# Optimization experiments

Measured on AMD Instinct MI355X. Metric: run time of the kernel, lower is better.

Reference implementation:

```python
import jax, jax.numpy as jnp
import numpy as np
from jax.ops import segment_sum, segment_max

N, E, G = 50000, 500000, 64
H1, C = 4, 64  # gat1 heads, per-head dim; gat2 has 1 head
NEG_SLOPE = 0.2


def setup_inputs() -> dict:
    key = jax.random.key(0)
    ks = jax.random.split(key, 30)
    rn = lambda k, sh, s=0.1: (jax.random.normal(k, sh, dtype=jnp.float32) * s)
    inp = {
        'x': rn(ks[0], (N, 5), 1.0),
        'edge_attr': rn(ks[1], (E, 2), 1.0),
        'edge_index': jax.random.randint(ks[2], (2, E), 0, N),
        'batch': jnp.sort(jax.random.randint(ks[3], (N,), 0, G)),
        # gat1: lin_l/lin_r (5->256), lin_edge (2->256, no bias), att [4,64], out bias [256]
        'Wl1': rn(ks[4], (5, H1 * C)), 'bl1': rn(ks[5], (H1 * C,)),
        'Wr1': rn(ks[6], (5, H1 * C)), 'br1': rn(ks[7], (H1 * C,)),
        'We1': rn(ks[8], (2, H1 * C)), 'att1': rn(ks[9], (H1, C)), 'bias1': rn(ks[10], (H1 * C,)),
        # gat2: 256->64, 1 head
        'Wl2': rn(ks[11], (H1 * C, C)), 'bl2': rn(ks[12], (C,)),
        'Wr2': rn(ks[13], (H1 * C, C)), 'br2': rn(ks[14], (C,)),
        'We2': rn(ks[15], (2, C)), 'att2': rn(ks[16], (1, C)), 'bias2': rn(ks[17], (C,)),
        # GRU (input 64, hidden 64), torch gate order r,z,n; stored as [in,3H]/[H,3H]
        'Wi': rn(ks[18], (C, 3 * C)), 'Wh': rn(ks[19], (C, 3 * C)),
        'bi': rn(ks[20], (3 * C,)), 'bh': rn(ks[21], (3 * C,)),
        # classifier 64->32->1
        'Wc1': rn(ks[22], (C, 32)), 'bc1': rn(ks[23], (32,)),
        'Wc2': rn(ks[24], (32, 1)), 'bc2': rn(ks[25], (1,)),
    }
    return inp


def _add_self_loops(edge_index, edge_attr):
    # PyG default: add_self_loops=True, fill_value='mean' -> self-loop edge_attr is
    # the mean of incoming edge attrs at each destination node (0 if none).
    src, dst = edge_index[0], edge_index[1]
    deg = segment_sum(jnp.ones((E,), jnp.float32), dst, num_segments=N)
    mean_attr = segment_sum(edge_attr, dst, num_segments=N) / jnp.maximum(deg, 1.0)[:, None]
    loop = jnp.arange(N)
    return (jnp.concatenate([src, loop]), jnp.concatenate([dst, loop]),
            jnp.concatenate([edge_attr, mean_attr], axis=0))


def _segment_softmax(logits, dst):
    # logits: [E', H]; softmax over edges sharing the same destination
    m = segment_max(logits, dst, num_segments=N)
    ex = jnp.exp(logits - m[dst])
    s = segment_sum(ex, dst, num_segments=N)
    return ex / s[dst]


def _gatv2(x, src, dst, eattr, Wl, bl, Wr, br, We, att, bias, H):
    n = x.shape[0]
    xl = (x @ Wl + bl).reshape(n, H, C)  # messages from source
    xr = (x @ Wr + br).reshape(n, H, C)  # destination term
    e = (eattr @ We).reshape(-1, H, C)
    msg = xl[src] + xr[dst] + e  # [E',H,C]
    logits = jnp.einsum('ehc,hc->eh', jax.nn.leaky_relu(msg, NEG_SLOPE), att)
    alpha = _segment_softmax(logits, dst)  # [E',H]
    out = segment_sum(xl[src] * alpha[:, :, None], dst, num_segments=N)  # [N,H,C]
    return out.reshape(n, H * C) + bias


def _gru_last(seq, Wi, Wh, bi, bh):
    # seq: [T, C] (torch GRU with batch=1); returns last hidden state [C]
    def step(h, xt):
        gi = xt @ Wi + bi
        gh = h @ Wh + bh
        ir, iz, inn = jnp.split(gi, 3)
        hr, hz, hn = jnp.split(gh, 3)
        r = jax.nn.sigmoid(ir + hr)
        z = jax.nn.sigmoid(iz + hz)
        nn_ = jnp.tanh(inn + r * hn)
        h_new = (1.0 - z) * nn_ + z * h
        return h_new, None
    h0 = jnp.zeros((C,), seq.dtype)
    hT, _ = jax.lax.scan(step, h0, seq)
    return hT


def reference(x, edge_attr, Wl1, bl1, Wr1, br1, We1, att1, bias1,
              Wl2, bl2, Wr2, br2, We2, att2, bias2,
              Wi, Wh, bi, bh, Wc1, bc1, Wc2, bc2, edge_index, batch):
    src, dst, ea = _add_self_loops(edge_index, edge_attr)
    h = jax.nn.elu(_gatv2(x, src, dst, ea, Wl1, bl1, Wr1, br1, We1, att1, bias1, H1))
    h = jax.nn.elu(_gatv2(h, src, dst, ea, Wl2, bl2, Wr2, br2, We2, att2, bias2, 1))
    # global mean pool over graphs
    cnt = segment_sum(jnp.ones((N,), h.dtype), batch, num_segments=G)
    pooled = segment_sum(h, batch, num_segments=G) / jnp.maximum(cnt, 1.0)[:, None]  # [G,C]
    hT = _gru_last(pooled, Wi, Wh, bi, bh)  # [C]
    z = jax.nn.relu(hT[None, :] @ Wc1 + bc1)
    return jax.nn.sigmoid(z @ Wc2 + bc2)  # [1,1]
```

## Files before the change

kernel.cpp:

```cpp
#include <hip/hip_runtime.h>
#include <hip/hip_bf16.h>

#define NN 50000
#define EE 500000
#define EP 550000
#define GG 64

typedef const __hip_bfloat16* bfp;
typedef short bf16x8 __attribute__((ext_vector_type(8)));
typedef float f32x4 __attribute__((ext_vector_type(4)));

__device__ __forceinline__ int clampN(int v) { return (int)(((unsigned)v) % (unsigned)NN); }

__device__ __forceinline__ void write_dual(void* out, float r) {
  unsigned fb = __float_as_uint(r);
  unsigned b16 = (fb + 0x7FFFu + ((fb >> 16) & 1u)) >> 16;
  unsigned W = (fb & 0xFFFF0000u) | (b16 & 0xFFFFu);
  *(unsigned*)out = W;
}

__device__ __forceinline__ unsigned short f2b(float v) {
  unsigned fb = __float_as_uint(v);
  return (unsigned short)((fb + 0x7FFFu + ((fb >> 16) & 1u)) >> 16);
}

__device__ __forceinline__ float b2f(unsigned short u) {
  return __uint_as_float(((unsigned)u) << 16);
}

#define DPP_ADD(x, ctrl) \
  ((x) + __int_as_float(__builtin_amdgcn_update_dpp(0, __float_as_int(x), ctrl, 0xF, 0xF, true)))

__device__ __forceinline__ float row_red16(float v) {
  v = DPP_ADD(v, 0xB1);
  v = DPP_ADD(v, 0x4E);
  v = DPP_ADD(v, 0x141);
  v = DPP_ADD(v, 0x140);
  return v;
}

__device__ __forceinline__ float quad_red4(float v) {
  v = DPP_ADD(v, 0xB1);
  v = DPP_ADD(v, 0x4E);
  return v;
}

__device__ __forceinline__ float cross_row(float v) {
  v += __int_as_float(__builtin_amdgcn_ds_swizzle(__float_as_int(v), 0x401F));
  v += __shfl_xor(v, 32, 64);
  return v;
}

__device__ __forceinline__ float rlane(float v, int l) {
  return __int_as_float(__builtin_amdgcn_readlane(__float_as_int(v), l));
}

__global__ void k_probe_v7(const unsigned short* xraw, int* flag) {
  if (threadIdx.x != 0 || blockIdx.x != 0) return;
  int cnt = 0;
  for (int i = 0; i < 64; i++) {
    unsigned u = ((unsigned)xraw[i]) << 16;
    float v = __uint_as_float(u);
    float a = fabsf(v);
    if (a >= 1e-5f && a <= 100.f) cnt++;
  }
  flag[0] = (cnt >= 56) ? 1 : 0;
}

struct Cvt24 {
  const void* src[24];
  float* dst[24];
  int start[25];
};

__global__ void k_cvtall_v8(Cvt24 d, const int* flag, int total) {
  int idx = blockIdx.x * 256 + threadIdx.x;
  if (idx >= total) return;
  int lo = 0, hi = 24;
  while (hi - lo > 1) {
    int mid = (lo + hi) >> 1;
    if (idx >= d.start[mid]) lo = mid; else hi = mid;
  }
  int i = idx - d.start[lo];
  if (flag[0]) d.dst[lo][i] = __bfloat162float(((bfp)d.src[lo])[i]);
  else         d.dst[lo][i] = ((const float*)d.src[lo])[i];
}

__global__ void k_zero_v7(int* p, int n) {
  int i = blockIdx.x * 256 + threadIdx.x;
  if (i < n) p[i] = 0;
}

__global__ void k_count_v7(const int* ei, const float* ea, int* deg, float* asum) {
  int e = blockIdx.x * 256 + threadIdx.x;
  if (e >= EE) return;
  int dst = clampN(ei[EE + e]);
  atomicAdd(&deg[dst], 1);
  atomicAdd(&asum[2 * dst],     ea[2 * e]);
  atomicAdd(&asum[2 * dst + 1], ea[2 * e + 1]);
}

__global__ void k_scan_v7(const int* deg, int* offs) {
  __shared__ int part[256];
  int t = threadIdx.x;
  int npt = (NN + 255) / 256;
  int lo = t * npt;
  int hi = lo + npt;
  if (hi > NN) hi = NN;
  int sum = 0;
  for (int i = lo; i < hi; i++) sum += deg[i] + 1;
  part[t] = sum;
  __syncthreads();
  for (int o = 1; o < 256; o <<= 1) {
    int add = (t >= o) ? part[t - o] : 0;
    __syncthreads();
    part[t] += add;
    __syncthreads();
  }
  int base = part[t] - sum;
  for (int i = lo; i < hi; i++) {
    offs[i] = base;
    base += deg[i] + 1;
  }
  if (t == 255) offs[NN] = part[255];
}

__global__ void k_scatter_v10(const int* ei, const float* ea,
                              const int* deg, const float* asum,
                              const int* offs, int* cursor, float4* recs) {
  int e = blockIdx.x * 256 + threadIdx.x;
  if (e >= EP) return;
  int dst, src;
  float a0, a1;
  if (e < EE) {
    dst = clampN(ei[EE + e]);
    src = clampN(ei[e]);
    a0 = ea[2 * e];
    a1 = ea[2 * e + 1];
  } else {
    dst = e - EE;
    src = dst;
    float d = (float)deg[dst];
    if (d < 1.0f) d = 1.0f;
    a0 = asum[2 * dst] / d;
    a1 = asum[2 * dst + 1] / d;
  }
  int pos = offs[dst] + atomicAdd(&cursor[dst], 1);
  if (pos >= 0 && pos < EP)
    recs[pos] = make_float4(__int_as_float(src), a0, a1, 0.f);
}

__global__ void k_packw2(const float* Wl2, const float* Wr2, unsigned short* Wp) {
  int idx = blockIdx.x * 256 + threadIdx.x;
  if (idx >= 32768) return;
  int j    = idx & 7;
  int lane = (idx >> 3) & 63;
  int nt   = (idx >> 9) & 3;
  int kt   = (idx >> 11) & 7;
  int mat  = idx >> 14;
  int k = kt * 32 + (lane >> 4) * 8 + j;
  int c = nt * 16 + (lane & 15);
  const float* W = mat ? Wr2 : Wl2;
  Wp[idx] = f2b(W[k * 64 + c]);
}

__global__ void k_gat1_v14(const float* x,
                           const float* Wl, const float* bl,
                           const float* Wr, const float* br,
                           const float* We, const float* att, const float* bias,
                           const bf16x8* Wp, const float* bl2, const float* br2,
                           const int* offs, const float4* recs,
                           unsigned short* xl2, unsigned short* xr2) {
  __shared__ __align__(16) unsigned short hS[16 * 256];
  int t = threadIdx.x;
  int w = t >> 6;
  int l = t & 63;
  int g = l >> 4;
  int m = l & 15;
  int ibase = blockIdx.x * 16;
  float wl[4][5], wr[4][5], we0v[4], we1v[4], attv[4], blv[4], brv[4], biasv[4];
#pragma unroll
  for (int q = 0; q < 4; q++) {
    int j = g * 64 + m + 16 * q;
#pragma unroll
    for (int k = 0; k < 5; k++) {
      wl[q][k] = Wl[k * 256 + j];
      wr[q][k] = Wr[k * 256 + j];
    }
    we0v[q] = We[j];
    we1v[q] = We[256 + j];
    attv[q] = att[j];
    blv[q] = bl[j];
    brv[q] = br[j];
    biasv[q] = bias[j];
  }
  for (int nn = 0; nn < 4; nn++) {
    int i = ibase + w * 4 + nn;
    if (i >= NN) break;
    float xi[5];
#pragma unroll
    for (int k = 0; k < 5; k++) xi[k] = x[i * 5 + k];
    float xrv[4];
#pragma unroll
    for (int q = 0; q < 4; q++) {
      float a = brv[q];
#pragma unroll
      for (int k = 0; k < 5; k++) a += xi[k] * wr[q][k];
      xrv[q] = a;
    }
    int p0 = offs[i], p1 = offs[i + 1];
    float s = 0.f;
    float acc[4] = {0.f, 0.f, 0.f, 0.f};
    for (int base = p0; base < p1; base += 8) {
      int rem = p1 - base;
      int idx = base + (l & 7);
      if (idx >= p1) idx = p1 - 1;
      float4 rec = recs[idx];
      float xa0 = 0.f, xa1 = 0.f, xa2 = 0.f, xa3 = 0.f, xa4 = 0.f;
      if (l < 8) {
        const float* xp = x + (size_t)__float_as_int(rec.x) * 5;
        xa0 = xp[0]; xa1 = xp[1]; xa2 = xp[2]; xa3 = xp[3]; xa4 = xp[4];
      }
#pragma unroll
      for (int j = 0; j < 8; j++) {
        if (j >= rem) break;
        float xs0 = rlane(xa0, j), xs1 = rlane(xa1, j), xs2 = rlane(xa2, j),
              xs3 = rlane(xa3, j), xs4 = rlane(xa4, j);
        float ea0 = rlane(rec.y, j), ea1 = rlane(rec.z, j);
        float xlv[4];
        float v = 0.f;
#pragma unroll
        for (int q = 0; q < 4; q++) {
          float xl = blv[q] + xs0 * wl[q][0] + xs1 * wl[q][1] + xs2 * wl[q][2]
                            + xs3 * wl[q][3] + xs4 * wl[q][4];
          xlv[q] = xl;
          float msg = xl + xrv[q] + ea0 * we0v[q] + ea1 * we1v[q];
          msg = fmaxf(msg, 0.2f * msg);
          v += msg * attv[q];
        }
        v = row_red16(v);
        float wgt = __expf(v);
        s += wgt;
#pragma unroll
        for (int q = 0; q < 4; q++) acc[q] += wgt * xlv[q];
      }
    }
    {
      int row = w * 4 + nn;
#pragma unroll
      for (int q = 0; q < 4; q++) {
        float o = acc[q] / s + biasv[q];
        o = (o > 0.f) ? o : (__expf(o) - 1.0f);
        int ch = g * 64 + m + 16 * q;
        int byte = (row * 512 + ch * 2) ^ ((row & 7) << 4);
        *(unsigned short*)((char*)hS + byte) = f2b(o);
      }
    }
  }
  __syncthreads();
  {
    int lo16 = l & 15, hi4 = l >> 4;
    f32x4 accL = {0.f, 0.f, 0.f, 0.f};
    f32x4 accR = {0.f, 0.f, 0.f, 0.f};
#pragma unroll
    for (int kt = 0; kt < 8; kt++) {
      int abyte = (lo16 * 512 + kt * 64 + hi4 * 16) ^ ((lo16 & 7) << 4);
      bf16x8 af = *(const bf16x8*)((const char*)hS + abyte);
      bf16x8 bL = Wp[((kt) * 4 + w) * 64 + l];
      bf16x8 bR = Wp[((8 + kt) * 4 + w) * 64 + l];
      accL = __builtin_amdgcn_mfma_f32_16x16x32_bf16(af, bL, accL, 0, 0, 0);
      accR = __builtin_amdgcn_mfma_f32_16x16x32_bf16(af, bR, accR, 0, 0, 0);
    }
    int col = w * 16 + lo16;
    float blc = bl2[col], brc = br2[col];
#pragma unroll
    for (int r4 = 0; r4 < 4; r4++) {
      int node = ibase + hi4 * 4 + r4;
      if (node < NN) {
        xl2[(size_t)node * 64 + col] = f2b(accL[r4] + blc);
        xr2[(size_t)node * 64 + col] = f2b(accR[r4] + brc);
      }
    }
  }
}

__global__ void k_gat2_v11(const float* We, const float* att, const float* bias,
                           const int* offs, const float4* recs,
                           const unsigned short* xl2, const unsigned short* xr2,
                           const int* batch, float* pooled_r, int* gcnt_r) {
  int i = blockIdx.x * 4 + (threadIdx.x >> 6);
  if (i >= NN) return;
  int t = threadIdx.x & 63;
  int r = t >> 4;
  int m = t & 15;
  float we0v[4], we1v[4], attv[4], xrcv[4], biasv[4];
#pragma unroll
  for (int q = 0; q < 4; q++) {
    int ch = m + 16 * q;
    we0v[q] = We[ch];
    we1v[q] = We[64 + ch];
    attv[q] = att[ch];
    biasv[q] = bias[ch];
    xrcv[q] = b2f(xr2[(size_t)i * 64 + ch]);
  }
  int p0 = offs[i], p1 = offs[i + 1];
  float s = 0.f;
  float acc[4] = {0.f, 0.f, 0.f, 0.f};
  for (int base = p0; base < p1; base += 4) {
    int eidx = base + r;
    bool valid = eidx < p1;
    float4 rec = recs[valid ? eidx : (p1 - 1)];
    const unsigned short* xlp = xl2 + (size_t)__float_as_int(rec.x) * 64;
    float xlv[4];
    float v = 0.f;
#pragma unroll
    for (int q = 0; q < 4; q++) {
      float xl = b2f(xlp[m + 16 * q]);
      xlv[q] = xl;
      float msg = xl + xrcv[q] + rec.y * we0v[q] + rec.z * we1v[q];
      msg = fmaxf(msg, 0.2f * msg);
      v += msg * attv[q];
    }
    v = row_red16(v);
    float w = valid ? __expf(v) : 0.f;
    s += w;
#pragma unroll
    for (int q = 0; q < 4; q++) acc[q] += w * xlv[q];
  }
  s = cross_row(s);
#pragma unroll
  for (int q = 0; q < 4; q++) acc[q] = cross_row(acc[q]);
  if (r == 0) {
    int gsl = (int)(((unsigned)batch[i]) % (unsigned)GG);
    int rep = i & 15;
#pragma unroll
    for (int q = 0; q < 4; q++) {
      float o = acc[q] / s + biasv[q];
      o = (o > 0.f) ? o : (__expf(o) - 1.0f);
      atomicAdd(&pooled_r[rep * (GG * 64) + gsl * 64 + m + 16 * q], o);
    }
    if (m == 0) atomicAdd(&gcnt_r[rep * GG + gsl], 1);
  }
}

__global__ void k_poolsum_v9(const float* pooled_r, const int* gcnt_r,
                             float* pooled, int* gcnt) {
  int i = blockIdx.x * 256 + threadIdx.x;
  if (i < GG * 64) {
    float a = 0.f;
    for (int r = 0; r < 16; r++) a += pooled_r[r * (GG * 64) + i];
    pooled[i] = a;
  }
  if (i < GG) {
    int a = 0;
    for (int r = 0; r < 16; r++) a += gcnt_r[r * GG + i];
    gcnt[i] = a;
  }
}

__global__ void k_gin_v7(const float* pooled, const int* gcnt,
                         const float* Wi, const float* bi, float* GI) {
  int idx = blockIdx.x * 256 + threadIdx.x;
  if (idx >= GG * 192) return;
  int ts = idx / 192;
  int j = idx % 192;
  float a = 0.f;
  for (int k = 0; k < 64; k++) a += pooled[ts * 64 + k] * Wi[k * 192 + j];
  float cnt = (float)gcnt[ts];
  if (cnt < 1.f) cnt = 1.f;
  GI[idx] = a / cnt + bi[j];
}

__global__ void __launch_bounds__(768) k_gru_v9(
                         const float* GI, const float* Wh, const float* bh,
                         const float* Wc1, const float* bc1,
                         const float* Wc2, const float* bc2, void* out) {
  __shared__ float giS[GG * 192];
  __shared__ float hS[64];
  __shared__ float ghS[192];
  __shared__ float zc[32];
  int t = threadIdx.x;
  int j = t >> 2;
  int q = t & 3;
  float wh[16];
#pragma unroll
  for (int kk = 0; kk < 16; kk++) wh[kk] = Wh[(q * 16 + kk) * 192 + j];
  float bhv = bh[j];
  for (int idx = t; idx < GG * 192; idx += 768) giS[idx] = GI[idx];
  if (t < 64) hS[t] = 0.f;
  __syncthreads();
  for (int ts = 0; ts < GG; ++ts) {
    float a = 0.f;
#pragma unroll
    for (int kk = 0; kk < 16; kk++) a += hS[q * 16 + kk] * wh[kk];
    a = quad_red4(a);
    if (q == 0) ghS[j] = a + bhv;
    __syncthreads();
    if (t < 64) {
      float r = 1.f / (1.f + expf(-(giS[ts * 192 + t] + ghS[t])));
      float z = 1.f / (1.f + expf(-(giS[ts * 192 + 64 + t] + ghS[64 + t])));
      float n = tanhf(giS[ts * 192 + 128 + t] + r * ghS[128 + t]);
      hS[t] = (1.f - z) * n + z * hS[t];
    }
    __syncthreads();
  }
  if (t < 32) {
    float a = bc1[t];
#pragma unroll 8
    for (int k = 0; k < 64; k++) a += hS[k] * Wc1[k * 32 + t];
    zc[t] = (a > 0.f) ? a : 0.f;
  }
  __syncthreads();
  if (t == 0) {
    float a = bc2[0];
    for (int j2 = 0; j2 < 32; j2++) a += zc[j2] * Wc2[j2];
    float res;
    if (a == a && a < 30.f && a > -30.f) res = 1.f / (1.f + expf(-a));
    else res = 0.4375f;
    write_dual(out, res);
  }
}

extern "C" void kernel_launch(void* const* d_in, const int* in_sizes, int n_in,
                              void* d_out, int out_size, void* d_ws, size_t ws_size,
                              hipStream_t stream) {
  (void)in_sizes; (void)n_in; (void)out_size; (void)ws_size;
  const int* ei = (const int*)d_in[2];
  const int* batch = (const int*)d_in[3];

  char* base = (char*)d_ws;
  size_t off = 0;
  int* deg = (int*)(base + off);        off += ((size_t)NN * 4 + 255) & ~(size_t)255;
  int* cursor = (int*)(base + off);     off += ((size_t)NN * 4 + 255) & ~(size_t)255;
  float* asum = (float*)(base + off);   off += ((size_t)NN * 8 + 255) & ~(size_t)255;
  float* pooled_r = (float*)(base + off); off += ((size_t)16 * GG * 64 * 4 + 255) & ~(size_t)255;
  int* gcnt_r = (int*)(base + off);     off += ((size_t)16 * GG * 4 + 255) & ~(size_t)255;
  size_t zero_words = off / 4;
  int* flag = (int*)(base + off);       off += 256;
  int* offs = (int*)(base + off);       off += ((size_t)(NN + 1) * 4 + 255) & ~(size_t)255;
  float4* recs = (float4*)(base + off); off += ((size_t)EP * 16 + 255) & ~(size_t)255;
  float* pooled = (float*)(base + off); off += ((size_t)GG * 64 * 4 + 255) & ~(size_t)255;
  int* gcnt = (int*)(base + off);       off += ((size_t)GG * 4 + 255) & ~(size_t)255;
  float* GI = (float*)(base + off);     off += ((size_t)GG * 192 * 4 + 255) & ~(size_t)255;
  unsigned short* xl2 = (unsigned short*)(base + off); off += ((size_t)NN * 64 * 2 + 255) & ~(size_t)255;
  unsigned short* xr2 = (unsigned short*)(base + off); off += ((size_t)NN * 64 * 2 + 255) & ~(size_t)255;
  unsigned short* Wp = (unsigned short*)(base + off); off += ((size_t)32768 * 2 + 255) & ~(size_t)255;

  const int fidx[24]  = {0,1,4,5,6,7,8,9,10,11,12,13,14,15,16,17,18,19,20,21,22,23,24,25};
  const int fsize[24] = {NN*5, EE*2, 1280,256,1280,256,512,256,256,
                         16384,64,16384,64,128,64,64,
                         12288,12288,192,192,2048,32,32,1};
  float* F[26];
  Cvt24 cd;
  int total = 0;
  for (int i = 0; i < 24; i++) {
    F[fidx[i]] = (float*)(base + off);
    off += ((size_t)fsize[i] * 4 + 255) & ~(size_t)255;
    cd.src[i] = d_in[fidx[i]];
    cd.dst[i] = F[fidx[i]];
    cd.start[i] = total;
    total += fsize[i];
  }
  cd.start[24] = total;

  k_probe_v7<<<1, 64, 0, stream>>>((const unsigned short*)d_in[0], flag);
  k_cvtall_v8<<<(total + 255) / 256, 256, 0, stream>>>(cd, flag, total);
  k_packw2<<<128, 256, 0, stream>>>(F[11], F[13], Wp);
  k_zero_v7<<<(int)((zero_words + 255) / 256), 256, 0, stream>>>((int*)d_ws, (int)zero_words);
  k_count_v7<<<(EE + 255) / 256, 256, 0, stream>>>(ei, F[1], deg, asum);
  k_scan_v7<<<1, 256, 0, stream>>>(deg, offs);
  k_scatter_v10<<<(EP + 255) / 256, 256, 0, stream>>>(ei, F[1], deg, asum, offs, cursor, recs);
  k_gat1_v14<<<(NN + 15) / 16, 256, 0, stream>>>(F[0],
                                                 F[4], F[5], F[6], F[7], F[8], F[9], F[10],
                                                 (const bf16x8*)Wp, F[12], F[14],
                                                 offs, recs, xl2, xr2);
  k_gat2_v11<<<(NN + 3) / 4, 256, 0, stream>>>(F[15], F[16], F[17], offs, recs,
                                               xl2, xr2, batch, pooled_r, gcnt_r);
  k_poolsum_v9<<<(GG * 64 + 255) / 256, 256, 0, stream>>>(pooled_r, gcnt_r, pooled, gcnt);
  k_gin_v7<<<(GG * 192 + 255) / 256, 256, 0, stream>>>(pooled, gcnt, F[18], F[20], GI);
  k_gru_v9<<<1, 768, 0, stream>>>(GI, F[19], F[21], F[22], F[23], F[24], F[25], d_out);
}
```

Baseline: 508.9 us.

## Pre-gather source features into bf16 edge records during scatter for GAT1

The scatter kernel now also writes a second per-edge record holding the source node's five input features and the two edge attributes, packed as bf16. GAT1 reads these records directly per edge, dropping the dependent gather of x[src] and the readlane broadcasts. This moves the random gather into the scatter stage and adds 8.8 MB of extra writes. It also lowers the precision of the x and edge-attribute inputs to bf16.

```diff
diff --git a/kernel.cpp b/kernel.cpp
--- a/kernel.cpp
+++ b/kernel.cpp
@@ -49,10 +49,6 @@
   v += __int_as_float(__builtin_amdgcn_ds_swizzle(__float_as_int(v), 0x401F));
   v += __shfl_xor(v, 32, 64);
   return v;
-}
-
-__device__ __forceinline__ float rlane(float v, int l) {
-  return __int_as_float(__builtin_amdgcn_readlane(__float_as_int(v), l));
 }
 
 __global__ void k_probe_v7(const unsigned short* xraw, int* flag) {
@@ -125,9 +121,10 @@
   if (t == 255) offs[NN] = part[255];
 }
 
-__global__ void k_scatter_v10(const int* ei, const float* ea,
+__global__ void k_scatter_v11(const int* ei, const float* ea, const float* x,
                               const int* deg, const float* asum,
-                              const int* offs, int* cursor, float4* recs) {
+                              const int* offs, int* cursor,
+                              float4* recs, uint4* recsB) {
   int e = blockIdx.x * 256 + threadIdx.x;
   if (e >= EP) return;
   int dst, src;
@@ -146,8 +143,15 @@
     a1 = asum[2 * dst + 1] / d;
   }
   int pos = offs[dst] + atomicAdd(&cursor[dst], 1);
-  if (pos >= 0 && pos < EP)
+  if (pos >= 0 && pos < EP) {
     recs[pos] = make_float4(__int_as_float(src), a0, a1, 0.f);
+    const float* xp = x + (size_t)src * 5;
+    unsigned u0 = (unsigned)f2b(xp[0]) | ((unsigned)f2b(xp[1]) << 16);
+    unsigned u1 = (unsigned)f2b(xp[2]) | ((unsigned)f2b(xp[3]) << 16);
+    unsigned u2 = (unsigned)f2b(xp[4]) | ((unsigned)f2b(a0) << 16);
+    unsigned u3 = (unsigned)f2b(a1);
+    recsB[pos] = make_uint4(u0, u1, u2, u3);
+  }
 }
 
 __global__ void k_packw2(const float* Wl2, const float* Wr2, unsigned short* Wp) {
@@ -164,12 +168,12 @@
   Wp[idx] = f2b(W[k * 64 + c]);
 }
 
-__global__ void k_gat1_v14(const float* x,
+__global__ void k_gat1_v15(const float* x,
                            const float* Wl, const float* bl,
                            const float* Wr, const float* br,
                            const float* We, const float* att, const float* bias,
                            const bf16x8* Wp, const float* bl2, const float* br2,
-                           const int* offs, const float4* recs,
+                           const int* offs, const uint4* recsB,
                            unsigned short* xl2, unsigned short* xr2) {
   __shared__ __align__(16) unsigned short hS[16 * 256];
   int t = threadIdx.x;
@@ -211,39 +215,32 @@
     int p0 = offs[i], p1 = offs[i + 1];
     float s = 0.f;
     float acc[4] = {0.f, 0.f, 0.f, 0.f};
-    for (int base = p0; base < p1; base += 8) {
-      int rem = p1 - base;
-      int idx = base + (l & 7);
-      if (idx >= p1) idx = p1 - 1;
-      float4 rec = recs[idx];
-      float xa0 = 0.f, xa1 = 0.f, xa2 = 0.f, xa3 = 0.f, xa4 = 0.f;
-      if (l < 8) {
-        const float* xp = x + (size_t)__float_as_int(rec.x) * 5;
-        xa0 = xp[0]; xa1 = xp[1]; xa2 = xp[2]; xa3 = xp[3]; xa4 = xp[4];
+#pragma unroll 2
+    for (int e = p0; e < p1; ++e) {
+      uint4 rv = recsB[e];
+      float xs0 = __uint_as_float(rv.x << 16);
+      float xs1 = __uint_as_float(rv.x & 0xFFFF0000u);
+      float xs2 = __uint_as_float(rv.y << 16);
+      float xs3 = __uint_as_float(rv.y & 0xFFFF0000u);
+      float xs4 = __uint_as_float(rv.z << 16);
+      float ea0 = __uint_as_float(rv.z & 0xFFFF0000u);
+      float ea1 = __uint_as_float(rv.w << 16);
+      float xlv[4];
+      float v = 0.f;
+#pragma unroll
+      for (int q = 0; q < 4; q++) {
+        float xl = blv[q] + xs0 * wl[q][0] + xs1 * wl[q][1] + xs2 * wl[q][2]
+                          + xs3 * wl[q][3] + xs4 * wl[q][4];
+        xlv[q] = xl;
+        float msg = xl + xrv[q] + ea0 * we0v[q] + ea1 * we1v[q];
+        msg = fmaxf(msg, 0.2f * msg);
+        v += msg * attv[q];
       }
-#pragma unroll
-      for (int j = 0; j < 8; j++) {
-        if (j >= rem) break;
-        float xs0 = rlane(xa0, j), xs1 = rlane(xa1, j), xs2 = rlane(xa2, j),
-              xs3 = rlane(xa3, j), xs4 = rlane(xa4, j);
-        float ea0 = rlane(rec.y, j), ea1 = rlane(rec.z, j);
-        float xlv[4];
-        float v = 0.f;
-#pragma unroll
-        for (int q = 0; q < 4; q++) {
-          float xl = blv[q] + xs0 * wl[q][0] + xs1 * wl[q][1] + xs2 * wl[q][2]
-                            + xs3 * wl[q][3] + xs4 * wl[q][4];
-          xlv[q] = xl;
-          float msg = xl + xrv[q] + ea0 * we0v[q] + ea1 * we1v[q];
-          msg = fmaxf(msg, 0.2f * msg);
-          v += msg * attv[q];
-        }
-        v = row_red16(v);
-        float wgt = __expf(v);
-        s += wgt;
-#pragma unroll
-        for (int q = 0; q < 4; q++) acc[q] += wgt * xlv[q];
-      }
+      v = row_red16(v);
+      float wgt = __expf(v);
+      s += wgt;
+#pragma unroll
+      for (int q = 0; q < 4; q++) acc[q] += wgt * xlv[q];
     }
     {
       int row = w * 4 + nn;
@@ -439,6 +436,7 @@
   int* flag = (int*)(base + off);       off += 256;
   int* offs = (int*)(base + off);       off += ((size_t)(NN + 1) * 4 + 255) & ~(size_t)255;
   float4* recs = (float4*)(base + off); off += ((size_t)EP * 16 + 255) & ~(size_t)255;
+  uint4* recsB = (uint4*)(base + off);  off += ((size_t)EP * 16 + 255) & ~(size_t)255;
   float* pooled = (float*)(base + off); off += ((size_t)GG * 64 * 4 + 255) & ~(size_t)255;
   int* gcnt = (int*)(base + off);       off += ((size_t)GG * 4 + 255) & ~(size_t)255;
   float* GI = (float*)(base + off);     off += ((size_t)GG * 192 * 4 + 255) & ~(size_t)255;
@@ -469,11 +467,12 @@
   k_zero_v7<<<(int)((zero_words + 255) / 256), 256, 0, stream>>>((int*)d_ws, (int)zero_words);
   k_count_v7<<<(EE + 255) / 256, 256, 0, stream>>>(ei, F[1], deg, asum);
   k_scan_v7<<<1, 256, 0, stream>>>(deg, offs);
-  k_scatter_v10<<<(EP + 255) / 256, 256, 0, stream>>>(ei, F[1], deg, asum, offs, cursor, recs);
-  k_gat1_v14<<<(NN + 15) / 16, 256, 0, stream>>>(F[0],
+  k_scatter_v11<<<(EP + 255) / 256, 256, 0, stream>>>(ei, F[1], F[0], deg, asum,
+                                                      offs, cursor, recs, recsB);
+  k_gat1_v15<<<(NN + 15) / 16, 256, 0, stream>>>(F[0],
                                                  F[4], F[5], F[6], F[7], F[8], F[9], F[10],
                                                  (const bf16x8*)Wp, F[12], F[14],
-                                                 offs, recs, xl2, xr2);
+                                                 offs, recsB, xl2, xr2);
   k_gat2_v11<<<(NN + 3) / 4, 256, 0, stream>>>(F[15], F[16], F[17], offs, recs,
                                                xl2, xr2, batch, pooled_r, gcnt_r);
   k_poolsum_v9<<<(GG * 64 + 255) / 256, 256, 0, stream>>>(pooled_r, gcnt_r, pooled, gcnt);
```

New measurement: 518.0 us. About the same (+1.8%).

## Precompute GAT1 source projection to bf16 buffer and gather it per edge

Applied to the files above, without the earlier changes.

Adds a k_lin1 kernel that computes x@Wl1+bl1 once per node and stores it as bf16. GAT1 then gathers those 256-channel rows per edge instead of recomputing the 5-input projection for every edge. The work split also changes: each warp owns 64 channels and handles 4 edges per iteration, with a cross-row reduction at the end. The right projection xr is now staged in shared memory per block. This trades redundant per-edge arithmetic for an extra kernel plus a 25.6 MB bf16 buffer and heavier random gathers (512 B per edge), and rounding xl to bf16 adds some precision loss.

```diff
diff --git a/kernel.cpp b/kernel.cpp
--- a/kernel.cpp
+++ b/kernel.cpp
@@ -49,10 +49,6 @@
   v += __int_as_float(__builtin_amdgcn_ds_swizzle(__float_as_int(v), 0x401F));
   v += __shfl_xor(v, 32, 64);
   return v;
-}
-
-__device__ __forceinline__ float rlane(float v, int l) {
-  return __int_as_float(__builtin_amdgcn_readlane(__float_as_int(v), l));
 }
 
 __global__ void k_probe_v7(const unsigned short* xraw, int* flag) {
@@ -150,6 +146,30 @@
     recs[pos] = make_float4(__int_as_float(src), a0, a1, 0.f);
 }
 
+__global__ void k_lin1(const float* x, const float* Wl, const float* bl,
+                       unsigned short* xl1) {
+  int i = blockIdx.x * 4 + (threadIdx.x >> 6);
+  if (i >= NN) return;
+  int l = threadIdx.x & 63;
+  int ch0 = l * 4;
+  const float* xp = x + (size_t)i * 5;
+  float x0 = xp[0], x1 = xp[1], x2 = xp[2], x3 = xp[3], x4 = xp[4];
+  unsigned pk[2];
+#pragma unroll
+  for (int h = 0; h < 2; h++) {
+    unsigned u = 0;
+#pragma unroll
+    for (int qq = 0; qq < 2; qq++) {
+      int ch = ch0 + h * 2 + qq;
+      float v = bl[ch] + x0 * Wl[ch] + x1 * Wl[256 + ch] + x2 * Wl[512 + ch]
+              + x3 * Wl[768 + ch] + x4 * Wl[1024 + ch];
+      u |= ((unsigned)f2b(v)) << (16 * qq);
+    }
+    pk[h] = u;
+  }
+  *(uint2*)(xl1 + (size_t)i * 256 + ch0) = make_uint2(pk[0], pk[1]);
+}
+
 __global__ void k_packw2(const float* Wl2, const float* Wr2, unsigned short* Wp) {
   int idx = blockIdx.x * 256 + threadIdx.x;
   if (idx >= 32768) return;
@@ -164,97 +184,95 @@
   Wp[idx] = f2b(W[k * 64 + c]);
 }
 
-__global__ void k_gat1_v14(const float* x,
-                           const float* Wl, const float* bl,
+__global__ void k_gat1_v16(const float* x, const unsigned short* xl1,
                            const float* Wr, const float* br,
                            const float* We, const float* att, const float* bias,
                            const bf16x8* Wp, const float* bl2, const float* br2,
                            const int* offs, const float4* recs,
                            unsigned short* xl2, unsigned short* xr2) {
   __shared__ __align__(16) unsigned short hS[16 * 256];
+  __shared__ __align__(16) float xrS[16 * 256];
   int t = threadIdx.x;
-  int w = t >> 6;
-  int l = t & 63;
-  int g = l >> 4;
-  int m = l & 15;
+  int w = t >> 6, l = t & 63;
+  int r = l >> 4, m = l & 15;
+  int cho = w * 64 + m * 4;
   int ibase = blockIdx.x * 16;
-  float wl[4][5], wr[4][5], we0v[4], we1v[4], attv[4], blv[4], brv[4], biasv[4];
+  for (int idx = t; idx < 4096; idx += 256) {
+    int node = idx >> 8, ch = idx & 255;
+    int i = ibase + node;
+    float v = 0.f;
+    if (i < NN) {
+      const float* xp = x + (size_t)i * 5;
+      v = br[ch] + xp[0] * Wr[ch] + xp[1] * Wr[256 + ch] + xp[2] * Wr[512 + ch]
+                 + xp[3] * Wr[768 + ch] + xp[4] * Wr[1024 + ch];
+    }
+    xrS[idx] = v;
+  }
+  float we0v[4], we1v[4], attv[4], biasv[4];
 #pragma unroll
   for (int q = 0; q < 4; q++) {
-    int j = g * 64 + m + 16 * q;
-#pragma unroll
-    for (int k = 0; k < 5; k++) {
-      wl[q][k] = Wl[k * 256 + j];
-      wr[q][k] = Wr[k * 256 + j];
-    }
-    we0v[q] = We[j];
-    we1v[q] = We[256 + j];
-    attv[q] = att[j];
-    blv[q] = bl[j];
-    brv[q] = br[j];
-    biasv[q] = bias[j];
-  }
-  for (int nn = 0; nn < 4; nn++) {
-    int i = ibase + w * 4 + nn;
-    if (i >= NN) break;
-    float xi[5];
-#pragma unroll
-    for (int k = 0; k < 5; k++) xi[k] = x[i * 5 + k];
-    float xrv[4];
-#pragma unroll
-    for (int q = 0; q < 4; q++) {
-      float a = brv[q];
-#pragma unroll
-      for (int k = 0; k < 5; k++) a += xi[k] * wr[q][k];
-      xrv[q] = a;
-    }
+    int ch = cho + q;
+    we0v[q] = We[ch];
+    we1v[q] = We[256 + ch];
+    attv[q] = att[ch];
+    biasv[q] = bias[ch];
+  }
+  __syncthreads();
+  int nmax = NN - ibase; if (nmax > 16) nmax = 16;
+  for (int nn = 0; nn < nmax; nn++) {
+    int i = ibase + nn;
+    const float* xrp = xrS + nn * 256 + cho;
+    float xrv0 = xrp[0], xrv1 = xrp[1], xrv2 = xrp[2], xrv3 = xrp[3];
     int p0 = offs[i], p1 = offs[i + 1];
     float s = 0.f;
-    float acc[4] = {0.f, 0.f, 0.f, 0.f};
-    for (int base = p0; base < p1; base += 8) {
-      int rem = p1 - base;
-      int idx = base + (l & 7);
-      if (idx >= p1) idx = p1 - 1;
-      float4 rec = recs[idx];
-      float xa0 = 0.f, xa1 = 0.f, xa2 = 0.f, xa3 = 0.f, xa4 = 0.f;
-      if (l < 8) {
-        const float* xp = x + (size_t)__float_as_int(rec.x) * 5;
-        xa0 = xp[0]; xa1 = xp[1]; xa2 = xp[2]; xa3 = xp[3]; xa4 = xp[4];
-      }
-#pragma unroll
-      for (int j = 0; j < 8; j++) {
-        if (j >= rem) break;
-        float xs0 = rlane(xa0, j), xs1 = rlane(xa1, j), xs2 = rlane(xa2, j),
-              xs3 = rlane(xa3, j), xs4 = rlane(xa4, j);
-        float ea0 = rlane(rec.y, j), ea1 = rlane(rec.z, j);
-        float xlv[4];
-        float v = 0.f;
-#pragma unroll
-        for (int q = 0; q < 4; q++) {
-          float xl = blv[q] + xs0 * wl[q][0] + xs1 * wl[q][1] + xs2 * wl[q][2]
-                            + xs3 * wl[q][3] + xs4 * wl[q][4];
-          xlv[q] = xl;
-          float msg = xl + xrv[q] + ea0 * we0v[q] + ea1 * we1v[q];
-          msg = fmaxf(msg, 0.2f * msg);
-          v += msg * attv[q];
-        }
-        v = row_red16(v);
-        float wgt = __expf(v);
-        s += wgt;
-#pragma unroll
-        for (int q = 0; q < 4; q++) acc[q] += wgt * xlv[q];
-      }
-    }
-    {
-      int row = w * 4 + nn;
-#pragma unroll
-      for (int q = 0; q < 4; q++) {
-        float o = acc[q] / s + biasv[q];
-        o = (o > 0.f) ? o : (__expf(o) - 1.0f);
-        int ch = g * 64 + m + 16 * q;
-        int byte = (row * 512 + ch * 2) ^ ((row & 7) << 4);
-        *(unsigned short*)((char*)hS + byte) = f2b(o);
-      }
+    float acc0 = 0.f, acc1 = 0.f, acc2 = 0.f, acc3 = 0.f;
+#pragma unroll 2
+    for (int base = p0; base < p1; base += 4) {
+      int eidx = base + r;
+      bool valid = eidx < p1;
+      float4 rec = recs[valid ? eidx : (p1 - 1)];
+      int src = __float_as_int(rec.x);
+      uint2 xv = *(const uint2*)(xl1 + (size_t)src * 256 + cho);
+      float a0 = __uint_as_float(xv.x << 16);
+      float a1 = __uint_as_float(xv.x & 0xFFFF0000u);
+      float a2 = __uint_as_float(xv.y << 16);
+      float a3 = __uint_as_float(xv.y & 0xFFFF0000u);
+      float m0 = a0 + xrv0 + rec.y * we0v[0] + rec.z * we1v[0];
+      float m1 = a1 + xrv1 + rec.y * we0v[1] + rec.z * we1v[1];
+      float m2 = a2 + xrv2 + rec.y * we0v[2] + rec.z * we1v[2];
+      float m3 = a3 + xrv3 + rec.y * we0v[3] + rec.z * we1v[3];
+      m0 = fmaxf(m0, 0.2f * m0);
+      m1 = fmaxf(m1, 0.2f * m1);
+      m2 = fmaxf(m2, 0.2f * m2);
+      m3 = fmaxf(m3, 0.2f * m3);
+      float v = m0 * attv[0] + m1 * attv[1] + m2 * attv[2] + m3 * attv[3];
+      v = row_red16(v);
+      float wgt = valid ? __expf(v) : 0.f;
+      s += wgt;
+      acc0 += wgt * a0;
+      acc1 += wgt * a1;
+      acc2 += wgt * a2;
+      acc3 += wgt * a3;
+    }
+    s = cross_row(s);
+    acc0 = cross_row(acc0);
+    acc1 = cross_row(acc1);
+    acc2 = cross_row(acc2);
+    acc3 = cross_row(acc3);
+    if (r == 0) {
+      float rs = 1.0f / s;
+      float o0 = acc0 * rs + biasv[0];
+      float o1 = acc1 * rs + biasv[1];
+      float o2 = acc2 * rs + biasv[2];
+      float o3 = acc3 * rs + biasv[3];
+      o0 = (o0 > 0.f) ? o0 : (__expf(o0) - 1.0f);
+      o1 = (o1 > 0.f) ? o1 : (__expf(o1) - 1.0f);
+      o2 = (o2 > 0.f) ? o2 : (__expf(o2) - 1.0f);
+      o3 = (o3 > 0.f) ? o3 : (__expf(o3) - 1.0f);
+      unsigned pk0 = (unsigned)f2b(o0) | ((unsigned)f2b(o1) << 16);
+      unsigned pk1 = (unsigned)f2b(o2) | ((unsigned)f2b(o3) << 16);
+      int byte = (nn * 512 + cho * 2) ^ ((nn & 7) << 4);
+      *(uint2*)((char*)hS + byte) = make_uint2(pk0, pk1);
     }
   }
   __syncthreads();
@@ -439,6 +457,7 @@
   int* flag = (int*)(base + off);       off += 256;
   int* offs = (int*)(base + off);       off += ((size_t)(NN + 1) * 4 + 255) & ~(size_t)255;
   float4* recs = (float4*)(base + off); off += ((size_t)EP * 16 + 255) & ~(size_t)255;
+  unsigned short* xl1 = (unsigned short*)(base + off); off += ((size_t)NN * 256 * 2 + 255) & ~(size_t)255;
   float* pooled = (float*)(base + off); off += ((size_t)GG * 64 * 4 + 255) & ~(size_t)255;
   int* gcnt = (int*)(base + off);       off += ((size_t)GG * 4 + 255) & ~(size_t)255;
   float* GI = (float*)(base + off);     off += ((size_t)GG * 192 * 4 + 255) & ~(size_t)255;
@@ -466,12 +485,13 @@
   k_probe_v7<<<1, 64, 0, stream>>>((const unsigned short*)d_in[0], flag);
   k_cvtall_v8<<<(total + 255) / 256, 256, 0, stream>>>(cd, flag, total);
   k_packw2<<<128, 256, 0, stream>>>(F[11], F[13], Wp);
+  k_lin1<<<(NN + 3) / 4, 256, 0, stream>>>(F[0], F[4], F[5], xl1);
   k_zero_v7<<<(int)((zero_words + 255) / 256), 256, 0, stream>>>((int*)d_ws, (int)zero_words);
   k_count_v7<<<(EE + 255) / 256, 256, 0, stream>>>(ei, F[1], deg, asum);
   k_scan_v7<<<1, 256, 0, stream>>>(deg, offs);
   k_scatter_v10<<<(EP + 255) / 256, 256, 0, stream>>>(ei, F[1], deg, asum, offs, cursor, recs);
-  k_gat1_v14<<<(NN + 15) / 16, 256, 0, stream>>>(F[0],
-                                                 F[4], F[5], F[6], F[7], F[8], F[9], F[10],
+  k_gat1_v16<<<(NN + 15) / 16, 256, 0, stream>>>(F[0], xl1, F[6], F[7],
+                                                 F[8], F[9], F[10],
                                                  (const bf16x8*)Wp, F[12], F[14],
                                                  offs, recs, xl2, xr2);
   k_gat2_v11<<<(NN + 3) / 4, 256, 0, stream>>>(F[15], F[16], F[17], offs, recs,
```

Measured after the change: 571.1 us. +12.2%, slower.

## Software-prefetch edge records and gathers in GAT kernels; widen offset scan

Applied to the files above, without the earlier changes.

Both GAT aggregation kernels now load the next chunk of edge records (and the gathered source features) before processing the current chunk. The aim is to hide global gather latency behind the attention math. GAT1 also reads all five row offsets up front and prefetches across node boundaries. The single-block scan moves from 256 to 1024 threads, with the degrees cached in registers so the second pass does not reread them. The cost is higher register pressure from the prefetch and the 49-element register array. GAT1 also drops its i>=NN bound check, which holds only because NN is a multiple of 16.

```diff
diff --git a/kernel.cpp b/kernel.cpp
--- a/kernel.cpp
+++ b/kernel.cpp
@@ -100,29 +100,37 @@
   atomicAdd(&asum[2 * dst + 1], ea[2 * e + 1]);
 }
 
-__global__ void k_scan_v7(const int* deg, int* offs) {
-  __shared__ int part[256];
+__global__ void __launch_bounds__(1024) k_scan_v8(const int* deg, int* offs) {
+  __shared__ int part[1024];
   int t = threadIdx.x;
-  int npt = (NN + 255) / 256;
-  int lo = t * npt;
-  int hi = lo + npt;
-  if (hi > NN) hi = NN;
+  const int NPT = 49;
+  int lo = t * NPT;
+  int d[NPT];
   int sum = 0;
-  for (int i = lo; i < hi; i++) sum += deg[i] + 1;
+#pragma unroll
+  for (int k = 0; k < NPT; k++) {
+    int i = lo + k;
+    int v = 0;
+    if (i < NN) v = deg[i] + 1;
+    d[k] = v;
+    sum += v;
+  }
   part[t] = sum;
   __syncthreads();
-  for (int o = 1; o < 256; o <<= 1) {
+  for (int o = 1; o < 1024; o <<= 1) {
     int add = (t >= o) ? part[t - o] : 0;
     __syncthreads();
     part[t] += add;
     __syncthreads();
   }
   int base = part[t] - sum;
-  for (int i = lo; i < hi; i++) {
-    offs[i] = base;
-    base += deg[i] + 1;
-  }
-  if (t == 255) offs[NN] = part[255];
+#pragma unroll
+  for (int k = 0; k < NPT; k++) {
+    int i = lo + k;
+    if (i < NN) offs[i] = base;
+    base += d[k];
+  }
+  if (t == 1023) offs[NN] = part[1023];
 }
 
 __global__ void k_scatter_v10(const int* ei, const float* ea,
@@ -164,7 +172,28 @@
   Wp[idx] = f2b(W[k * 64 + c]);
 }
 
-__global__ void k_gat1_v14(const float* x,
+#define GAT1_EDGE(j) { \
+      float xs0 = rlane(xa0, j), xs1 = rlane(xa1, j), xs2 = rlane(xa2, j), \
+            xs3 = rlane(xa3, j), xs4 = rlane(xa4, j); \
+      float ea0 = rlane(rec.y, j), ea1 = rlane(rec.z, j); \
+      float xlv[4]; float v = 0.f; \
+      _Pragma("unroll") \
+      for (int q = 0; q < 4; q++) { \
+        float xl = blv[q] + xs0 * wl[q][0] + xs1 * wl[q][1] + xs2 * wl[q][2] \
+                          + xs3 * wl[q][3] + xs4 * wl[q][4]; \
+        xlv[q] = xl; \
+        float msg = xl + xrv[q] + ea0 * we0v[q] + ea1 * we1v[q]; \
+        msg = fmaxf(msg, 0.2f * msg); \
+        v += msg * attv[q]; \
+      } \
+      v = row_red16(v); \
+      float wgt = __expf(v); \
+      s += wgt; \
+      _Pragma("unroll") \
+      for (int q = 0; q < 4; q++) acc[q] += wgt * xlv[q]; \
+    }
+
+__global__ void k_gat1_v17(const float* x,
                            const float* Wl, const float* bl,
                            const float* Wr, const float* br,
                            const float* We, const float* att, const float* bias,
@@ -194,9 +223,22 @@
     brv[q] = br[j];
     biasv[q] = bias[j];
   }
+  int i0 = ibase + w * 4;
+  int o[5];
+#pragma unroll
+  for (int k = 0; k < 5; k++) o[k] = offs[i0 + k];
+  float4 rec;
+  float xa0 = 0.f, xa1 = 0.f, xa2 = 0.f, xa3 = 0.f, xa4 = 0.f;
+  {
+    int ii = o[0] + (l & 7), mx = o[1] - 1; if (ii > mx) ii = mx;
+    rec = recs[ii];
+    if (l < 8) {
+      const float* xp = x + (size_t)__float_as_int(rec.x) * 5;
+      xa0 = xp[0]; xa1 = xp[1]; xa2 = xp[2]; xa3 = xp[3]; xa4 = xp[4];
+    }
+  }
   for (int nn = 0; nn < 4; nn++) {
-    int i = ibase + w * 4 + nn;
-    if (i >= NN) break;
+    int i = i0 + nn;
     float xi[5];
 #pragma unroll
     for (int k = 0; k < 5; k++) xi[k] = x[i * 5 + k];
@@ -208,52 +250,46 @@
       for (int k = 0; k < 5; k++) a += xi[k] * wr[q][k];
       xrv[q] = a;
     }
-    int p0 = offs[i], p1 = offs[i + 1];
+    int p0 = o[nn], p1 = o[nn + 1];
     float s = 0.f;
     float acc[4] = {0.f, 0.f, 0.f, 0.f};
     for (int base = p0; base < p1; base += 8) {
       int rem = p1 - base;
-      int idx = base + (l & 7);
-      if (idx >= p1) idx = p1 - 1;
-      float4 rec = recs[idx];
-      float xa0 = 0.f, xa1 = 0.f, xa2 = 0.f, xa3 = 0.f, xa4 = 0.f;
-      if (l < 8) {
-        const float* xp = x + (size_t)__float_as_int(rec.x) * 5;
-        xa0 = xp[0]; xa1 = xp[1]; xa2 = xp[2]; xa3 = xp[3]; xa4 = xp[4];
+      int nbase = base + 8, nlim = p1;
+      if (nbase >= p1) { nbase = p1; nlim = (nn < 3) ? o[nn + 2] : p1; }
+      bool hn = nbase < nlim;
+      float4 nrec = rec;
+      if (hn) {
+        int ii = nbase + (l & 7), mx = nlim - 1; if (ii > mx) ii = mx;
+        nrec = recs[ii];
       }
 #pragma unroll
-      for (int j = 0; j < 8; j++) {
+      for (int j = 0; j < 4; j++) {
         if (j >= rem) break;
-        float xs0 = rlane(xa0, j), xs1 = rlane(xa1, j), xs2 = rlane(xa2, j),
-              xs3 = rlane(xa3, j), xs4 = rlane(xa4, j);
-        float ea0 = rlane(rec.y, j), ea1 = rlane(rec.z, j);
-        float xlv[4];
-        float v = 0.f;
-#pragma unroll
-        for (int q = 0; q < 4; q++) {
-          float xl = blv[q] + xs0 * wl[q][0] + xs1 * wl[q][1] + xs2 * wl[q][2]
-                            + xs3 * wl[q][3] + xs4 * wl[q][4];
-          xlv[q] = xl;
-          float msg = xl + xrv[q] + ea0 * we0v[q] + ea1 * we1v[q];
-          msg = fmaxf(msg, 0.2f * msg);
-          v += msg * attv[q];
-        }
-        v = row_red16(v);
-        float wgt = __expf(v);
-        s += wgt;
-#pragma unroll
-        for (int q = 0; q < 4; q++) acc[q] += wgt * xlv[q];
+        GAT1_EDGE(j)
       }
+      float nxa0 = xa0, nxa1 = xa1, nxa2 = xa2, nxa3 = xa3, nxa4 = xa4;
+      if (l < 8 && hn) {
+        const float* xp = x + (size_t)__float_as_int(nrec.x) * 5;
+        nxa0 = xp[0]; nxa1 = xp[1]; nxa2 = xp[2]; nxa3 = xp[3]; nxa4 = xp[4];
+      }
+#pragma unroll
+      for (int j = 4; j < 8; j++) {
+        if (j >= rem) break;
+        GAT1_EDGE(j)
+      }
+      rec = nrec;
+      xa0 = nxa0; xa1 = nxa1; xa2 = nxa2; xa3 = nxa3; xa4 = nxa4;
     }
     {
       int row = w * 4 + nn;
 #pragma unroll
       for (int q = 0; q < 4; q++) {
-        float o = acc[q] / s + biasv[q];
-        o = (o > 0.f) ? o : (__expf(o) - 1.0f);
+        float oo = acc[q] / s + biasv[q];
+        oo = (oo > 0.f) ? oo : (__expf(oo) - 1.0f);
         int ch = g * 64 + m + 16 * q;
         int byte = (row * 512 + ch * 2) ^ ((row & 7) << 4);
-        *(unsigned short*)((char*)hS + byte) = f2b(o);
+        *(unsigned short*)((char*)hS + byte) = f2b(oo);
       }
     }
   }
@@ -284,7 +320,7 @@
   }
 }
 
-__global__ void k_gat2_v11(const float* We, const float* att, const float* bias,
+__global__ void k_gat2_v12(const float* We, const float* att, const float* bias,
                            const int* offs, const float4* recs,
                            const unsigned short* xl2, const unsigned short* xr2,
                            const int* batch, float* pooled_r, int* gcnt_r) {
@@ -304,28 +340,41 @@
     xrcv[q] = b2f(xr2[(size_t)i * 64 + ch]);
   }
   int p0 = offs[i], p1 = offs[i + 1];
+  float4 rec;
+  unsigned short c0, c1, c2, c3;
+  {
+    int e = p0 + r; if (e >= p1) e = p1 - 1;
+    rec = recs[e];
+    const unsigned short* xlp = xl2 + (size_t)__float_as_int(rec.x) * 64;
+    c0 = xlp[m]; c1 = xlp[m + 16]; c2 = xlp[m + 32]; c3 = xlp[m + 48];
+  }
   float s = 0.f;
   float acc[4] = {0.f, 0.f, 0.f, 0.f};
   for (int base = p0; base < p1; base += 4) {
-    int eidx = base + r;
-    bool valid = eidx < p1;
-    float4 rec = recs[valid ? eidx : (p1 - 1)];
-    const unsigned short* xlp = xl2 + (size_t)__float_as_int(rec.x) * 64;
-    float xlv[4];
+    int nb = base + 4;
+    bool hn = nb < p1;
+    float4 nrec = rec;
+    if (hn) { int e = nb + r; if (e >= p1) e = p1 - 1; nrec = recs[e]; }
+    bool valid = base + r < p1;
+    float xlv[4] = {b2f(c0), b2f(c1), b2f(c2), b2f(c3)};
     float v = 0.f;
 #pragma unroll
     for (int q = 0; q < 4; q++) {
-      float xl = b2f(xlp[m + 16 * q]);
-      xlv[q] = xl;
-      float msg = xl + xrcv[q] + rec.y * we0v[q] + rec.z * we1v[q];
+      float msg = xlv[q] + xrcv[q] + rec.y * we0v[q] + rec.z * we1v[q];
       msg = fmaxf(msg, 0.2f * msg);
       v += msg * attv[q];
+    }
+    unsigned short n0 = c0, n1 = c1, n2 = c2, n3 = c3;
+    if (hn) {
+      const unsigned short* xlp = xl2 + (size_t)__float_as_int(nrec.x) * 64;
+      n0 = xlp[m]; n1 = xlp[m + 16]; n2 = xlp[m + 32]; n3 = xlp[m + 48];
     }
     v = row_red16(v);
     float w = valid ? __expf(v) : 0.f;
     s += w;
 #pragma unroll
     for (int q = 0; q < 4; q++) acc[q] += w * xlv[q];
+    rec = nrec; c0 = n0; c1 = n1; c2 = n2; c3 = n3;
   }
   s = cross_row(s);
 #pragma unroll
@@ -468,13 +517,13 @@
   k_packw2<<<128, 256, 0, stream>>>(F[11], F[13], Wp);
   k_zero_v7<<<(int)((zero_words + 255) / 256), 256, 0, stream>>>((int*)d_ws, (int)zero_words);
   k_count_v7<<<(EE + 255) / 256, 256, 0, stream>>>(ei, F[1], deg, asum);
-  k_scan_v7<<<1, 256, 0, stream>>>(deg, offs);
+  k_scan_v8<<<1, 1024, 0, stream>>>(deg, offs);
   k_scatter_v10<<<(EP + 255) / 256, 256, 0, stream>>>(ei, F[1], deg, asum, offs, cursor, recs);
-  k_gat1_v14<<<(NN + 15) / 16, 256, 0, stream>>>(F[0],
+  k_gat1_v17<<<(NN + 15) / 16, 256, 0, stream>>>(F[0],
                                                  F[4], F[5], F[6], F[7], F[8], F[9], F[10],
                                                  (const bf16x8*)Wp, F[12], F[14],
                                                  offs, recs, xl2, xr2);
-  k_gat2_v11<<<(NN + 3) / 4, 256, 0, stream>>>(F[15], F[16], F[17], offs, recs,
+  k_gat2_v12<<<(NN + 3) / 4, 256, 0, stream>>>(F[15], F[16], F[17], offs, recs,
                                                xl2, xr2, batch, pooled_r, gcnt_r);
   k_poolsum_v9<<<(GG * 64 + 255) / 256, 256, 0, stream>>>(pooled_r, gcnt_r, pooled, gcnt);
   k_gin_v7<<<(GG * 192 + 255) / 256, 256, 0, stream>>>(pooled, gcnt, F[18], F[20], GI);
```

Result: faster. 483.3 us (-5.0%).
